# Kernel optimization log

Measured on AMD Instinct MI355X. Metric: run time of the kernel, lower is better.

The kernel has to match this reference:

```python
import jax, jax.numpy as jnp
import numpy as np

INV_COEFF = 25.0
VAR_COEFF = 25.0
COV_COEFF = 1.0


def _cdist(a, b):
    # Euclidean pairwise distance, (B,N,C)x(B,M,C)->(B,N,M)
    a2 = jnp.sum(a * a, axis=-1)[:, :, None]
    b2 = jnp.sum(b * b, axis=-1)[:, None, :]
    d2 = a2 + b2 - 2.0 * jnp.einsum('bnc,bmc->bnm', a, b)
    return jnp.sqrt(jnp.maximum(d2, 0.0))


def _nn_match(input_maps, candidate_maps, distances, num_matches):
    # top-1 NN per input row, then keep the num_matches rows with the
    # smallest NN-distance, preserving original row order (matches the
    # torch sort/sort/mask + masked_select logic exactly).
    min_vals = jnp.min(distances, axis=-1)       # (B, N)
    nn_idx = jnp.argmin(distances, axis=-1)      # (B, N)
    order = jnp.argsort(min_vals, axis=1)[:, :num_matches]   # rows with smallest min-dist
    indices_selected = jnp.sort(order, axis=1)               # restore original order (B, M)
    nn_selected = jnp.take_along_axis(nn_idx, indices_selected, axis=1)  # (B, M)
    filt_in = jnp.take_along_axis(input_maps, indices_selected[..., None], axis=1)
    filt_cand = jnp.take_along_axis(candidate_maps, nn_selected[..., None], axis=1)
    return filt_in, filt_cand


def _vicreg_loss(x, y):
    # x, y: (B, M, C)
    B = x.shape[0]
    C = x.shape[-1]
    repr_loss = INV_COEFF * jnp.mean((x - y) ** 2)
    # gather_center: subtract batch mean (single-device equivalent)
    xc = x - jnp.mean(x, axis=0, keepdims=True)
    yc = y - jnp.mean(y, axis=0, keepdims=True)
    std_x = jnp.sqrt(jnp.var(xc, axis=0, ddof=1) + 1e-4)
    std_y = jnp.sqrt(jnp.var(yc, axis=0, ddof=1) + 1e-4)
    std_loss = VAR_COEFF * (jnp.mean(jax.nn.relu(1.0 - std_x)) / 2
                            + jnp.mean(jax.nn.relu(1.0 - std_y)) / 2)
    # covariance per location: permute to (M, B, C), center over batch
    xp = jnp.transpose(xc, (1, 0, 2))
    yp = jnp.transpose(yc, (1, 0, 2))
    xp = xp - jnp.mean(xp, axis=-2, keepdims=True)
    yp = yp - jnp.mean(yp, axis=-2, keepdims=True)
    cov_x = jnp.einsum('mnc,mnd->mcd', xp, xp) / (B - 1)
    cov_y = jnp.einsum('mnc,mnd->mcd', yp, yp) / (B - 1)
    off = 1.0 - jnp.eye(C, dtype=x.dtype)
    cov_loss = (jnp.sum((cov_x * off) ** 2, axis=(-2, -1)) / C / 2
                + jnp.sum((cov_y * off) ** 2, axis=(-2, -1)) / C / 2)
    cov_loss = COV_COEFF * jnp.mean(cov_loss)
    return repr_loss, std_loss, cov_loss


def _local_loss(maps_1, maps_2, location_1, location_2, num_matches):
    # L2-feature-space NN matching, both directions
    m1f_l2, m1nn_l2 = _nn_match(maps_1, maps_2, _cdist(maps_1, maps_2), num_matches)
    m2f_l2, m2nn_l2 = _nn_match(maps_2, maps_1, _cdist(maps_2, maps_1), num_matches)
    # location-space NN matching, both directions
    loc1 = location_1.reshape(location_1.shape[0], -1, location_1.shape[-1])
    loc2 = location_2.reshape(location_2.shape[0], -1, location_2.shape[-1])
    m1f_loc, m1nn_loc = _nn_match(maps_1, maps_2, _cdist(loc1, loc2), num_matches)
    m2f_loc, m2nn_loc = _nn_match(maps_2, maps_1, _cdist(loc2, loc1), num_matches)
    inv = var = cov = 0.0
    for a, b in ((m1f_l2, m1nn_l2), (m2f_l2, m2nn_l2),
                 (m1f_loc, m1nn_loc), (m2f_loc, m2nn_loc)):
        i, v, c = _vicreg_loss(a, b)
        inv = inv + i
        var = var + v
        cov = cov + c
    return inv + var + cov


def setup_inputs() -> dict:
    key = jax.random.key(0)
    k1, k2, k3, k4 = jax.random.split(key, 4)
    B, HW, C, H = 64, 784, 512, 28
    return {
        'maps_1': jax.random.normal(k1, (B, HW, C), dtype=jnp.float32),
        'maps_2': jax.random.normal(k2, (B, HW, C), dtype=jnp.float32),
        'location_1': jax.random.uniform(k3, (B, H, H, 2), dtype=jnp.float32),
        'location_2': jax.random.uniform(k4, (B, H, H, 2), dtype=jnp.float32),
        'num_matches': 256,
    }


def reference(maps_1, maps_2, location_1, location_2, num_matches):
    return _local_loss(maps_1, maps_2, location_1, location_2, num_matches)
```

## Files before the change

kernel.cpp:

```cpp
#include <hip/hip_runtime.h>
#include <stdint.h>

#define B 64
#define N 784
#define C 512
#define M 256

typedef unsigned long long u64;
typedef unsigned short u16;
typedef __attribute__((ext_vector_type(8))) short short8;
typedef __attribute__((ext_vector_type(4))) float f32x4;

static __device__ __forceinline__ u64 umin64(u64 a, u64 b) { return a < b ? a : b; }

static __device__ __forceinline__ u16 f2bf(float x) {
    unsigned u = __float_as_uint(x);
    return (u16)((u + 0x7FFFu + ((u >> 16) & 1u)) >> 16);
}
static __device__ __forceinline__ float b2f(u16 v) {
    return __uint_as_float((unsigned)v << 16);
}

static __device__ __forceinline__ void gload_lds16(const u16* g, u16* l) {
    __builtin_amdgcn_global_load_lds((const __attribute__((address_space(1))) void*)g,
                                     (__attribute__((address_space(3))) void*)l, 16, 0, 0);
}

__global__ __launch_bounds__(256) void convnorm_kernel(
    const float* __restrict__ m1, const float* __restrict__ m2,
    u16* __restrict__ abf, u16* __restrict__ bbf, float* __restrict__ nrm,
    u64* __restrict__ rowkey) {
    int gid = blockIdx.x * 256 + threadIdx.x;
    if (gid < 2 * B * N) rowkey[gid] = ~0ull;
    int w = blockIdx.x * 4 + (threadIdx.x >> 6);
    int lane = threadIdx.x & 63;
    if (w >= 2 * B * N) return;
    const float* src = (w < B * N) ? m1 : m2;
    u16* dst = (w < B * N) ? abf : bbf;
    int row = (w < B * N) ? w : w - B * N;
    const float4* p = (const float4*)(src + (size_t)row * C);
    u64* q = (u64*)(dst + (size_t)row * C);
    float s = 0.f;
#pragma unroll
    for (int i = 0; i < 2; ++i) {
        int idx = lane + i * 64;
        float4 v = p[idx];
        s += v.x * v.x + v.y * v.y + v.z * v.z + v.w * v.w;
        q[idx] = (u64)f2bf(v.x) | ((u64)f2bf(v.y) << 16) |
                 ((u64)f2bf(v.z) << 32) | ((u64)f2bf(v.w) << 48);
    }
#pragma unroll
    for (int off = 32; off > 0; off >>= 1) s += __shfl_down(s, off, 64);
    if (lane == 0) nrm[w] = s;
}

__global__ __launch_bounds__(256, 2) void feat_mfma_kernel(
    const u16* __restrict__ abf, const u16* __restrict__ bbf,
    const float* __restrict__ nrm, u64* __restrict__ rowkey) {
    int id = blockIdx.x;
    int xcd = id & 7;
    int q = id >> 3;
    int hi = q / 49, t49 = q - hi * 49;
    int b = hi * 8 + xcd;
    int tn = t49 / 7, tm = t49 - tn * 7;

    const int t = threadIdx.x;
    const int lane = t & 63, wv = t >> 6;
    const int wr = wv >> 1, wc = wv & 1;

    __shared__ __align__(16) unsigned char RAW[65536];
    __shared__ float sNa[128], sNb[128];

    const int row0 = tn * 128, col0 = tm * 128;
    if (t < 128) {
        int n = row0 + t;
        sNa[t] = (n < N) ? nrm[b * N + n] : __builtin_inff();
    } else {
        int m = col0 + (t - 128);
        sNb[t - 128] = (m < N) ? nrm[B * N + b * N + m] : __builtin_inff();
    }

    size_t aofs[4], bofs[4];
    int ldso[4];
#pragma unroll
    for (int s = 0; s < 4; ++s) {
        int c = (wv * 4 + s) * 64 + lane;
        int rl = c >> 3;
        int grp = (c & 7) ^ (rl & 7);
        int ga = row0 + rl; if (ga > N - 1) ga = N - 1;
        int gb = col0 + rl; if (gb > N - 1) gb = N - 1;
        aofs[s] = ((size_t)b * N + ga) * C + grp * 8;
        bofs[s] = ((size_t)b * N + gb) * C + grp * 8;
        ldso[s] = (wv * 4 + s) * 512;
    }

    const int l15 = lane & 15;
    const int sA_base = (wr * 64 + l15) * 64;
    const int sB_base = (wc * 64 + l15) * 64;
    const int swz0 = (((lane >> 4) + 0) ^ (l15 & 7)) << 3;
    const int swz1 = (((lane >> 4) + 4) ^ (l15 & 7)) << 3;

    f32x4 acc[4][4];
#pragma unroll
    for (int i = 0; i < 4; ++i)
#pragma unroll
        for (int j = 0; j < 4; ++j) acc[i][j] = (f32x4){0.f, 0.f, 0.f, 0.f};

    {
        u16* A0 = (u16*)RAW;
        u16* B0 = A0 + 8192;
#pragma unroll
        for (int s = 0; s < 4; ++s) {
            gload_lds16(abf + aofs[s], &A0[ldso[s]]);
            gload_lds16(bbf + bofs[s], &B0[ldso[s]]);
        }
    }

    for (int kt = 0; kt < 8; ++kt) {
        const int cur = kt & 1;
        if (kt < 7) {
            int ke = (kt + 1) * 64;
            u16* An = (u16*)(RAW + (cur ^ 1) * 32768);
            u16* Bn = An + 8192;
#pragma unroll
            for (int s = 0; s < 4; ++s) {
                gload_lds16(abf + aofs[s] + ke, &An[ldso[s]]);
                gload_lds16(bbf + bofs[s] + ke, &Bn[ldso[s]]);
            }
            asm volatile("s_waitcnt vmcnt(8)" ::: "memory");
        } else {
            asm volatile("s_waitcnt vmcnt(0)" ::: "memory");
        }
        __builtin_amdgcn_s_barrier();

        const u16* Als = (const u16*)(RAW + cur * 32768);
        const u16* Bls = Als + 8192;
        const u16* pA0 = Als + sA_base + swz0;
        const u16* pA1 = Als + sA_base + swz1;
        const u16* pB0 = Bls + sB_base + swz0;
        const u16* pB1 = Bls + sB_base + swz1;
#pragma unroll
        for (int ks = 0; ks < 2; ++ks) {
            const u16* pA = ks ? pA1 : pA0;
            const u16* pB = ks ? pB1 : pB0;
            short8 afr[4], bfr[4];
#pragma unroll
            for (int f = 0; f < 4; ++f) {
                afr[f] = *(const short8*)(pA + f * 1024);
                bfr[f] = *(const short8*)(pB + f * 1024);
            }
#pragma unroll
            for (int fi = 0; fi < 4; ++fi)
#pragma unroll
                for (int fj = 0; fj < 4; ++fj)
                    acc[fi][fj] = __builtin_amdgcn_mfma_f32_16x16x32_bf16(
                        afr[fi], bfr[fj], acc[fi][fj], 0, 0, 0);
        }
        asm volatile("s_waitcnt lgkmcnt(0)" ::: "memory");
        __builtin_amdgcn_s_barrier();
    }

    const int g4 = (lane >> 4) << 2;
    float na4[4][4], nb4[4];
#pragma unroll
    for (int fi = 0; fi < 4; ++fi) {
        float4 v = *(const float4*)&sNa[wr * 64 + fi * 16 + g4];
        na4[fi][0] = v.x; na4[fi][1] = v.y; na4[fi][2] = v.z; na4[fi][3] = v.w;
    }
#pragma unroll
    for (int fj = 0; fj < 4; ++fj) nb4[fj] = sNb[wc * 64 + fj * 16 + l15];

    u64(*red)[33] = (u64(*)[33])RAW;
    u64 ck[4] = {~0ull, ~0ull, ~0ull, ~0ull};
#pragma unroll
    for (int fi = 0; fi < 4; ++fi) {
        int rl = wr * 64 + fi * 16 + g4;
        u64 rk[4] = {~0ull, ~0ull, ~0ull, ~0ull};
#pragma unroll
        for (int fj = 0; fj < 4; ++fj) {
            unsigned colidx = (unsigned)(col0 + wc * 64 + fj * 16 + l15);
#pragma unroll
            for (int reg = 0; reg < 4; ++reg) {
                float d2 = fmaxf(na4[fi][reg] + nb4[fj] - 2.f * acc[fi][fj][reg], 0.f);
                u64 hv = ((u64)__float_as_uint(d2) << 32);
                rk[reg] = umin64(rk[reg], hv | colidx);
                ck[fj] = umin64(ck[fj], hv | (unsigned)(row0 + rl + reg));
            }
        }
#pragma unroll
        for (int reg = 0; reg < 4; ++reg)
            red[rl + reg][(wc << 4) | l15] = rk[reg];
    }
#pragma unroll
    for (int fj = 0; fj < 4; ++fj) {
        u64 best = ck[fj];
        best = umin64(best, __shfl_xor(best, 16, 64));
        best = umin64(best, __shfl_xor(best, 32, 64));
        if (lane < 16) {
            int m = col0 + wc * 64 + fj * 16 + lane;
            if (m < N) atomicMin(&rowkey[(size_t)B * N + (size_t)b * N + m], best);
        }
    }
    __syncthreads();
    if (t < 128) {
        u64 best = red[t][0];
#pragma unroll
        for (int x = 1; x < 32; ++x) best = umin64(best, red[t][x]);
        int n = row0 + t;
        if (n < N) atomicMin(&rowkey[(size_t)b * N + n], best);
    }
}

__global__ __launch_bounds__(256) void loc_dist_kernel(
    const float* __restrict__ l1, const float* __restrict__ l2,
    u64* __restrict__ rowkey) {
    const int dir = blockIdx.z;
    const int b = blockIdx.y;
    const int t = threadIdx.x;
    const int n = blockIdx.x * 256 + t;
    __shared__ __align__(16) float4 s4[N];
    const float* Ap = dir ? l2 : l1;
    const float* Bp = dir ? l1 : l2;
    for (int i = t; i < N; i += 256) {
        float2 qv = ((const float2*)Bp)[b * N + i];
        s4[i] = make_float4(qv.x, qv.y, qv.x * qv.x + qv.y * qv.y, 0.f);
    }
    __syncthreads();
    if (n >= N) return;
    float2 a = ((const float2*)Ap)[b * N + n];
    float a2 = a.x * a.x + a.y * a.y;
    float nax = -2.f * a.x, nay = -2.f * a.y;
    u64 best = ~0ull;
#pragma unroll 4
    for (int mm = 0; mm < N; ++mm) {
        float4 v = s4[mm];
        float d2 = fmaxf(fmaf(nax, v.x, fmaf(nay, v.y, a2 + v.z)), 0.f);
        u64 kv = ((u64)__float_as_uint(d2) << 32) | (unsigned)mm;
        best = kv < best ? kv : best;
    }
    rowkey[(size_t)(2 + dir) * B * N + (size_t)b * N + n] = best;
}

__global__ __launch_bounds__(256) void select_kernel(
    const u64* __restrict__ rowkey, int* __restrict__ sel_idx,
    int* __restrict__ nn_idx, float* __restrict__ acc) {
    const int b = blockIdx.x;
    const int dir = blockIdx.y;
    const int t = threadIdx.x;
    if (b == 0 && dir == 0 && t < 8) acc[t] = 0.f;
    __shared__ u64 sk[1024];
    const u64* rk = rowkey + (size_t)dir * B * N + (size_t)b * N;
    for (int i = t; i < 1024; i += 256)
        sk[i] = (i < N) ? ((rk[i] & 0xFFFFFFFF00000000ull) | (unsigned)i) : ~0ull;
    __syncthreads();
    for (unsigned k = 2; k <= 1024; k <<= 1) {
        for (unsigned j = k >> 1; j > 0; j >>= 1) {
            for (unsigned i = t; i < 1024; i += 256) {
                unsigned ixj = i ^ j;
                if (ixj > i) {
                    u64 x = sk[i], y = sk[ixj];
                    bool up = ((i & k) == 0);
                    if ((x > y) == up) { sk[i] = y; sk[ixj] = x; }
                }
            }
            __syncthreads();
        }
    }
    unsigned myidx = (unsigned)(sk[t] & 0xFFFFFFFFull);
    __syncthreads();
    unsigned* si = (unsigned*)sk;
    si[t] = myidx;
    __syncthreads();
    for (unsigned k = 2; k <= 256; k <<= 1) {
        for (unsigned j = k >> 1; j > 0; j >>= 1) {
            unsigned i = t, ixj = i ^ j;
            if (ixj > i) {
                unsigned x = si[i], y = si[ixj];
                bool up = ((i & k) == 0);
                if ((x > y) == up) { si[i] = y; si[ixj] = x; }
            }
            __syncthreads();
        }
    }
    int sel = (int)si[t];
    sel_idx[((size_t)dir * B + b) * M + t] = sel;
    nn_idx[((size_t)dir * B + b) * M + t] = (int)(unsigned)(rk[sel] & 0xFFFFFFFFull);
}

__global__ __launch_bounds__(512, 1) void vicreg_mfma_kernel(
    const u16* __restrict__ abf, const u16* __restrict__ bbf,
    const int* __restrict__ sel_idx, const int* __restrict__ nn_idx,
    float* __restrict__ acc, float* __restrict__ outp) {
    const int mloc = blockIdx.x;
    const int p = blockIdx.y;
    const int t = threadIdx.x;
    const int l = t & 63, w = t >> 6;
    const int kh = w >> 2, wl = w & 3;

    __shared__ __align__(16) u16 Xs[4][64 * 128];
    __shared__ __align__(16) u16 Ys[4][64 * 128];
    __shared__ float colpart[2][4][4][128];
    __shared__ float Rsx[64], Rsy[64];
    __shared__ int xi[64], yi[64];
    __shared__ float redsc[4][4];

    if (t < 64) xi[t] = sel_idx[((size_t)p * B + t) * M + mloc];
    else if (t < 128) yi[t - 64] = nn_idx[((size_t)p * B + (t - 64)) * M + mloc];
    __syncthreads();

    const u16* Xg = (p & 1) ? bbf : abf;
    const u16* Yg = (p & 1) ? abf : bbf;
    unsigned xofs[4], yofs[4];
    int ldst[4];
#pragma unroll
    for (int s = 0; s < 4; ++s) {
        int r = wl * 16 + s * 4 + (l >> 4);
        int cs = (l & 15) ^ (r & 15);
        xofs[s] = (unsigned)((r * N + xi[r]) * C + cs * 8);
        yofs[s] = (unsigned)((r * N + yi[r]) * C + cs * 8);
        ldst[s] = (wl * 16 + s * 4) * 128;
    }

#pragma unroll
    for (int cc = 0; cc < 2; ++cc) {
        int kc = 2 * kh + cc;
#pragma unroll
        for (int s = 0; s < 4; ++s) {
            gload_lds16(Xg + xofs[s] + kc * 128, &Xs[kc][ldst[s]]);
            gload_lds16(Yg + yofs[s] + kc * 128, &Ys[kc][ldst[s]]);
        }
    }
    __syncthreads();

    f32x4 Gx[4], Gy[4], Z;
#pragma unroll
    for (int j = 0; j < 4; ++j) { Gx[j] = (f32x4){0,0,0,0}; Gy[j] = (f32x4){0,0,0,0}; }
    Z = (f32x4){0, 0, 0, 0};
    float stdacc = 0.f, covdacc = 0.f, reprp = 0.f;

#pragma unroll
    for (int cc = 0; cc < 2; ++cc) {
        const int kc = 2 * kh + cc;
        const u16* Xc = Xs[kc];
        const u16* Yc = Ys[kc];

#pragma unroll
        for (int ks = 0; ks < 4; ++ks) {
            int cb = ks * 4 + (l >> 4);
            int pe = (cb ^ (l & 15)) << 3;
            short8 ax = *(const short8*)&Xc[((wl << 4) + (l & 15)) * 128 + pe];
            short8 ay = *(const short8*)&Yc[((wl << 4) + (l & 15)) * 128 + pe];
            short8 bx[4], by[4];
#pragma unroll
            for (int j = 0; j < 4; ++j) {
                bx[j] = *(const short8*)&Xc[(j * 16 + (l & 15)) * 128 + pe];
                by[j] = *(const short8*)&Yc[(j * 16 + (l & 15)) * 128 + pe];
            }
#pragma unroll
            for (int j = 0; j < 4; ++j) {
                Gx[j] = __builtin_amdgcn_mfma_f32_16x16x32_bf16(ax, bx[j], Gx[j], 0, 0, 0);
                Gy[j] = __builtin_amdgcn_mfma_f32_16x16x32_bf16(ay, by[j], Gy[j], 0, 0, 0);
            }
            Z = __builtin_amdgcn_mfma_f32_16x16x32_bf16(ax, ay, Z, 0, 0, 0);
        }

        {
            int c4 = (l & 31) << 2;
            int cc8 = c4 >> 3, h = (c4 >> 2) & 1;
            int g2 = (wl << 1) + (l >> 5);
            float s1x0 = 0, s1x1 = 0, s1x2 = 0, s1x3 = 0;
            float s2x0 = 0, s2x1 = 0, s2x2 = 0, s2x3 = 0;
            float s1y0 = 0, s1y1 = 0, s1y2 = 0, s1y3 = 0;
            float s2y0 = 0, s2y1 = 0, s2y2 = 0, s2y3 = 0;
#pragma unroll
            for (int rr = 0; rr < 8; ++rr) {
                int r = g2 * 8 + rr;
                int off = r * 128 + ((cc8 ^ (r & 15)) << 3) + h * 4;
                ushort4 vx = *(const ushort4*)&Xc[off];
                ushort4 vy = *(const ushort4*)&Yc[off];
                float x0 = b2f(vx.x), x1 = b2f(vx.y), x2 = b2f(vx.z), x3 = b2f(vx.w);
                float y0 = b2f(vy.x), y1 = b2f(vy.y), y2 = b2f(vy.z), y3 = b2f(vy.w);
                s1x0 += x0; s1x1 += x1; s1x2 += x2; s1x3 += x3;
                s2x0 = fmaf(x0, x0, s2x0); s2x1 = fmaf(x1, x1, s2x1);
                s2x2 = fmaf(x2, x2, s2x2); s2x3 = fmaf(x3, x3, s2x3);
                s1y0 += y0; s1y1 += y1; s1y2 += y2; s1y3 += y3;
                s2y0 = fmaf(y0, y0, s2y0); s2y1 = fmaf(y1, y1, s2y1);
                s2y2 = fmaf(y2, y2, s2y2); s2y3 = fmaf(y3, y3, s2y3);
            }
            s1x0 += __shfl_xor(s1x0, 32, 64); s1x1 += __shfl_xor(s1x1, 32, 64);
            s1x2 += __shfl_xor(s1x2, 32, 64); s1x3 += __shfl_xor(s1x3, 32, 64);
            s2x0 += __shfl_xor(s2x0, 32, 64); s2x1 += __shfl_xor(s2x1, 32, 64);
            s2x2 += __shfl_xor(s2x2, 32, 64); s2x3 += __shfl_xor(s2x3, 32, 64);
            s1y0 += __shfl_xor(s1y0, 32, 64); s1y1 += __shfl_xor(s1y1, 32, 64);
            s1y2 += __shfl_xor(s1y2, 32, 64); s1y3 += __shfl_xor(s1y3, 32, 64);
            s2y0 += __shfl_xor(s2y0, 32, 64); s2y1 += __shfl_xor(s2y1, 32, 64);
            s2y2 += __shfl_xor(s2y2, 32, 64); s2y3 += __shfl_xor(s2y3, 32, 64);
            if (l < 32) {
                *(float4*)&colpart[kh][wl][0][c4] = make_float4(s1x0, s1x1, s1x2, s1x3);
                *(float4*)&colpart[kh][wl][1][c4] = make_float4(s2x0, s2x1, s2x2, s2x3);
                *(float4*)&colpart[kh][wl][2][c4] = make_float4(s1y0, s1y1, s1y2, s1y3);
                *(float4*)&colpart[kh][wl][3][c4] = make_float4(s2y0, s2y1, s2y2, s2y3);
            }
        }
        __syncthreads();

        if (t < 256) {
            int khp = t >> 7, col = t & 127;
            float s1x = 0, s2x = 0, s1y = 0, s2y = 0;
#pragma unroll
            for (int ww = 0; ww < 4; ++ww) {
                s1x += colpart[khp][ww][0][col]; s2x += colpart[khp][ww][1][col];
                s1y += colpart[khp][ww][2][col]; s2y += colpart[khp][ww][3][col];
            }
            float sx = s2x - s1x * s1x * (1.f / 64.f);
            float sy = s2y - s1y * s1y * (1.f / 64.f);
            stdacc += fmaxf(0.f, 1.f - sqrtf(sx * (1.f / 63.f) + 1e-4f)) +
                      fmaxf(0.f, 1.f - sqrtf(sy * (1.f / 63.f) + 1e-4f));
            covdacc += sx * sx + sy * sy;
            reprp += s2x + s2y;
        }
        __syncthreads();
    }

    {
        float* ex = (float*)&Xs[0][0];
        int base = ((wl << 6) + l) * 36;
        if (kh == 1) {
#pragma unroll
            for (int j = 0; j < 4; ++j)
#pragma unroll
                for (int reg = 0; reg < 4; ++reg) {
                    ex[base + j * 4 + reg] = Gx[j][reg];
                    ex[base + 16 + j * 4 + reg] = Gy[j][reg];
                }
#pragma unroll
            for (int reg = 0; reg < 4; ++reg) ex[base + 32 + reg] = Z[reg];
        }
        __syncthreads();
        if (kh == 0) {
#pragma unroll
            for (int j = 0; j < 4; ++j)
#pragma unroll
                for (int reg = 0; reg < 4; ++reg) {
                    Gx[j][reg] += ex[base + j * 4 + reg];
                    Gy[j][reg] += ex[base + 16 + j * 4 + reg];
                }
#pragma unroll
            for (int reg = 0; reg < 4; ++reg) Z[reg] += ex[base + 32 + reg];
        }
    }

    float zd = 0.f;
    float rsx[4] = {0, 0, 0, 0}, rsy[4] = {0, 0, 0, 0};
    if (kh == 0) {
        int rbase = (l >> 4) << 2, col = l & 15;
#pragma unroll
        for (int reg = 0; reg < 4; ++reg)
            zd += (col == rbase + reg) ? Z[reg] : 0.f;
#pragma unroll
        for (int reg = 0; reg < 4; ++reg) {
            rsx[reg] = Gx[0][reg] + Gx[1][reg] + Gx[2][reg] + Gx[3][reg];
            rsy[reg] = Gy[0][reg] + Gy[1][reg] + Gy[2][reg] + Gy[3][reg];
        }
#pragma unroll
        for (int off = 1; off < 16; off <<= 1)
#pragma unroll
            for (int reg = 0; reg < 4; ++reg) {
                rsx[reg] += __shfl_xor(rsx[reg], off, 64);
                rsy[reg] += __shfl_xor(rsy[reg], off, 64);
            }
        if ((l & 15) == 0) {
#pragma unroll
            for (int reg = 0; reg < 4; ++reg) {
                Rsx[(wl << 4) + ((l >> 4) << 2) + reg] = rsx[reg];
                Rsy[(wl << 4) + ((l >> 4) << 2) + reg] = rsy[reg];
            }
        }
    }
    __syncthreads();
    if (kh == 0) {
        float myx = Rsx[l], myy = Rsy[l];
#pragma unroll
        for (int off = 1; off < 64; off <<= 1) {
            myx += __shfl_xor(myx, off, 64);
            myy += __shfl_xor(myy, off, 64);
        }
        float tX = myx * (1.f / 4096.f), tY = myy * (1.f / 4096.f);
        float kn = 0.f;
#pragma unroll
        for (int j = 0; j < 4; ++j) {
            float cX = Rsx[(j << 4) + (l & 15)] * (1.f / 64.f);
            float cY = Rsy[(j << 4) + (l & 15)] * (1.f / 64.f);
#pragma unroll
            for (int reg = 0; reg < 4; ++reg) {
                float K1 = Gx[j][reg] - rsx[reg] * (1.f / 64.f) - cX + tX;
                kn = fmaf(K1, K1, kn);
                float K2 = Gy[j][reg] - rsy[reg] * (1.f / 64.f) - cY + tY;
                kn = fmaf(K2, K2, kn);
            }
        }
        float v0 = reprp - 2.f * zd, v1 = stdacc, v2 = covdacc, v3 = kn;
#pragma unroll
        for (int off = 1; off < 64; off <<= 1) {
            v0 += __shfl_xor(v0, off, 64);
            v1 += __shfl_xor(v1, off, 64);
            v2 += __shfl_xor(v2, off, 64);
            v3 += __shfl_xor(v3, off, 64);
        }
        if (l == 0) { redsc[wl][0] = v0; redsc[wl][1] = v1;
                      redsc[wl][2] = v2; redsc[wl][3] = v3; }
    }
    __syncthreads();
    if (t == 0) {
        float r0 = 0, r1 = 0, r2 = 0, r3 = 0;
#pragma unroll
        for (int ww = 0; ww < 4; ++ww) {
            r0 += redsc[ww][0]; r1 += redsc[ww][1];
            r2 += redsc[ww][2]; r3 += redsc[ww][3];
        }
        atomicAdd(&acc[0], r0);
        atomicAdd(&acc[1], r1);
        atomicAdd(&acc[2], r3 - r2);
        __threadfence();
        unsigned old = atomicAdd((unsigned*)&acc[6], 1u);
        if (old == 4 * M - 1) {
            float a0 = atomicAdd(&acc[0], 0.f);
            float a1 = atomicAdd(&acc[1], 0.f);
            float a2 = atomicAdd(&acc[2], 0.f);
            float repr = 25.f * a0 / ((float)B * (float)M * (float)C);
            float stdl = 12.5f * a1 / ((float)M * (float)C);
            float cov = a2 / (63.f * 63.f * (float)C * 2.f) / (float)M;
            outp[0] = repr + stdl + cov;
        }
    }
}

__global__ __launch_bounds__(256) void init_kernel(u64* rowkey, float* acc) {
    int i = blockIdx.x * 256 + threadIdx.x;
    if (i < 4 * B * N) rowkey[i] = ~0ull;
    if (i < 8) acc[i] = 0.f;
}

__global__ __launch_bounds__(256) void norms_kernel(const float* __restrict__ m1,
                                                    const float* __restrict__ m2,
                                                    float* __restrict__ nrm) {
    int w = blockIdx.x * 4 + (threadIdx.x >> 6);
    int lane = threadIdx.x & 63;
    if (w >= 2 * B * N) return;
    const float* src = (w < B * N) ? m1 : m2;
    int row = (w < B * N) ? w : w - B * N;
    const float4* p = (const float4*)(src + (size_t)row * C);
    float s = 0.f;
#pragma unroll
    for (int i = 0; i < 2; ++i) {
        float4 v = p[lane + i * 64];
        s += v.x * v.x + v.y * v.y + v.z * v.z + v.w * v.w;
    }
#pragma unroll
    for (int off = 32; off > 0; off >>= 1) s += __shfl_down(s, off, 64);
    if (lane == 0) nrm[w] = s;
}

__global__ __launch_bounds__(256) void feat_dist_kernel(
    const float* __restrict__ m1, const float* __restrict__ m2,
    const float* __restrict__ nrm, u64* __restrict__ rowkey) {
    const int b = blockIdx.z;
    const int tn = blockIdx.x, tm = blockIdx.y;
    __shared__ float As[64][68];
    __shared__ float Bt[64][68];
    __shared__ u64 red[64][16];
    const int t = threadIdx.x;
    const int ty = t >> 4, tx = t & 15;
    float acc[4][4] = {};
    const float* A = m1 + (size_t)b * N * C;
    const float* Bm = m2 + (size_t)b * N * C;

    for (int k0 = 0; k0 < C; k0 += 64) {
#pragma unroll
        for (int it = 0; it < 4; ++it) {
            int idx = t + it * 256;
            int r = idx >> 4, cc = (idx & 15) << 2;
            int n = tn * 64 + r;
            float4 v = make_float4(0.f, 0.f, 0.f, 0.f);
            if (n < N) v = *(const float4*)(A + (size_t)n * C + k0 + cc);
            *(float4*)&As[r][cc] = v;
            int mm = tm * 64 + r;
            float4 w = make_float4(0.f, 0.f, 0.f, 0.f);
            if (mm < N) w = *(const float4*)(Bm + (size_t)mm * C + k0 + cc);
            Bt[cc + 0][r] = w.x; Bt[cc + 1][r] = w.y;
            Bt[cc + 2][r] = w.z; Bt[cc + 3][r] = w.w;
        }
        __syncthreads();
#pragma unroll 4
        for (int kq = 0; kq < 64; kq += 4) {
            float aa[4][4], bb[4][4];
#pragma unroll
            for (int i = 0; i < 4; ++i) {
                float4 v = *(const float4*)&As[ty * 4 + i][kq];
                aa[i][0] = v.x; aa[i][1] = v.y; aa[i][2] = v.z; aa[i][3] = v.w;
            }
#pragma unroll
            for (int qq = 0; qq < 4; ++qq) {
                float4 v = *(const float4*)&Bt[kq + qq][tx * 4];
                bb[qq][0] = v.x; bb[qq][1] = v.y; bb[qq][2] = v.z; bb[qq][3] = v.w;
            }
#pragma unroll
            for (int qq = 0; qq < 4; ++qq)
#pragma unroll
                for (int i = 0; i < 4; ++i)
#pragma unroll
                    for (int j = 0; j < 4; ++j)
                        acc[i][j] = fmaf(aa[i][qq], bb[qq][j], acc[i][j]);
        }
        __syncthreads();
    }

    u64 rk[4] = {~0ull, ~0ull, ~0ull, ~0ull};
    u64 ck[4] = {~0ull, ~0ull, ~0ull, ~0ull};
    const float* nr1 = nrm;
    const float* nr2 = nrm + B * N;
#pragma unroll
    for (int i = 0; i < 4; ++i) {
        int n = tn * 64 + ty * 4 + i;
        if (n >= N) continue;
        float a2 = nr1[b * N + n];
#pragma unroll
        for (int j = 0; j < 4; ++j) {
            int mm = tm * 64 + tx * 4 + j;
            if (mm >= N) continue;
            float b2 = nr2[b * N + mm];
            float d2 = a2 + b2 - 2.f * acc[i][j];
            unsigned vb = __float_as_uint(fmaxf(d2, 0.f));
            u64 kv = ((u64)vb << 32);
            rk[i] = umin64(rk[i], kv | (unsigned)mm);
            ck[j] = umin64(ck[j], kv | (unsigned)n);
        }
    }
#pragma unroll
    for (int i = 0; i < 4; ++i) red[ty * 4 + i][tx] = rk[i];
    __syncthreads();
    if (t < 64) {
        u64 best = red[t][0];
#pragma unroll
        for (int x = 1; x < 16; ++x) best = umin64(best, red[t][x]);
        int n = tn * 64 + t;
        if (n < N && best != ~0ull)
            atomicMin(&rowkey[(size_t)b * N + n], best);
    }
    __syncthreads();
#pragma unroll
    for (int j = 0; j < 4; ++j) red[tx * 4 + j][ty] = ck[j];
    __syncthreads();
    if (t < 64) {
        u64 best = red[t][0];
#pragma unroll
        for (int x = 1; x < 16; ++x) best = umin64(best, red[t][x]);
        int mm = tm * 64 + t;
        if (mm < N && best != ~0ull)
            atomicMin(&rowkey[(size_t)B * N + (size_t)b * N + mm], best);
    }
}

__device__ __forceinline__ float blockReduce(float v, float* redb, int t) {
    __syncthreads();
    redb[t] = v;
    __syncthreads();
    for (int s = 128; s > 0; s >>= 1) {
        if (t < s) redb[t] += redb[t + s];
        __syncthreads();
    }
    return redb[0];
}

__global__ __launch_bounds__(256) void vicreg_kernel(
    const float* __restrict__ m1, const float* __restrict__ m2,
    const int* __restrict__ sel_idx, const int* __restrict__ nn_idx,
    float* __restrict__ acc) {
    const int mloc = blockIdx.x;
    const int p = blockIdx.y;
    const int t = threadIdx.x;
    const float* X = (p & 1) ? m2 : m1;
    const float* Y = (p & 1) ? m1 : m2;
    __shared__ float Xs[64][65];
    __shared__ float Ys[64][65];
    __shared__ int xi[64], yi[64];
    __shared__ float pst[192][5];
    __shared__ float Rs[64];
    __shared__ float Tsh;
    __shared__ float redb[256];

    if (t < 64) {
        xi[t] = sel_idx[((size_t)p * B + t) * M + mloc];
        yi[t] = nn_idx[((size_t)p * B + t) * M + mloc];
    }
    __syncthreads();

    float Gx[4][4] = {}, Gy[4][4] = {};
    float stdx = 0, stdy = 0, covdx = 0, covdy = 0, repr = 0;
    const int i0 = (t >> 4) << 2, j0 = (t & 15) << 2;

    for (int c0 = 0; c0 < C; c0 += 64) {
#pragma unroll
        for (int it = 0; it < 4; ++it) {
            int fidx = t + it * 256;
            int r = fidx >> 4, cc = (fidx & 15) << 2;
            float4 v = *(const float4*)(X + ((size_t)r * N + xi[r]) * C + c0 + cc);
            Xs[r][cc] = v.x; Xs[r][cc + 1] = v.y; Xs[r][cc + 2] = v.z; Xs[r][cc + 3] = v.w;
            float4 w = *(const float4*)(Y + ((size_t)r * N + yi[r]) * C + c0 + cc);
            Ys[r][cc] = w.x; Ys[r][cc + 1] = w.y; Ys[r][cc + 2] = w.z; Ys[r][cc + 3] = w.w;
        }
        __syncthreads();
#pragma unroll 4
        for (int k = 0; k < 64; ++k) {
            float ax[4], bx[4], ay[4], by[4];
#pragma unroll
            for (int i = 0; i < 4; ++i) { ax[i] = Xs[i0 + i][k]; ay[i] = Ys[i0 + i][k]; }
#pragma unroll
            for (int j = 0; j < 4; ++j) { bx[j] = Xs[j0 + j][k]; by[j] = Ys[j0 + j][k]; }
#pragma unroll
            for (int i = 0; i < 4; ++i)
#pragma unroll
                for (int j = 0; j < 4; ++j) {
                    Gx[i][j] = fmaf(ax[i], bx[j], Gx[i][j]);
                    Gy[i][j] = fmaf(ay[i], by[j], Gy[i][j]);
                }
        }
        {
            float s1x = 0, s2x = 0, s1y = 0, s2y = 0, sxy = 0;
            int col = t & 63, g = t >> 6;
            for (int r = g * 16; r < g * 16 + 16; ++r) {
                float xv = Xs[r][col], yv = Ys[r][col];
                s1x += xv; s2x += xv * xv;
                s1y += yv; s2y += yv * yv;
                sxy += xv * yv;
            }
            if (g) {
                float* qq = pst[(g - 1) * 64 + col];
                qq[0] = s1x; qq[1] = s2x; qq[2] = s1y; qq[3] = s2y; qq[4] = sxy;
            }
            __syncthreads();
            if (g == 0) {
#pragma unroll
                for (int gg = 0; gg < 3; ++gg) {
                    float* qq = pst[gg * 64 + col];
                    s1x += qq[0]; s2x += qq[1]; s1y += qq[2]; s2y += qq[3]; sxy += qq[4];
                }
                float xb = s1x * (1.f / 64.f);
                float sx = s2x - 64.f * xb * xb;
                float yb = s1y * (1.f / 64.f);
                float sy = s2y - 64.f * yb * yb;
                stdx += fmaxf(0.f, 1.f - sqrtf(sx * (1.f / 63.f) + 1e-4f));
                stdy += fmaxf(0.f, 1.f - sqrtf(sy * (1.f / 63.f) + 1e-4f));
                covdx += sx * sx;
                covdy += sy * sy;
                repr += s2x + s2y - 2.f * sxy;
            }
            __syncthreads();
        }
    }

    float knx = 0.f, kny = 0.f;
    float (*Gs)[65] = (float(*)[65]) & Xs[0][0];
    __syncthreads();
#pragma unroll
    for (int i = 0; i < 4; ++i)
#pragma unroll
        for (int j = 0; j < 4; ++j) Gs[i0 + i][j0 + j] = Gx[i][j];
    __syncthreads();
    if (t < 64) {
        float r = 0;
        for (int j = 0; j < 64; ++j) r += Gs[t][j];
        Rs[t] = r;
    }
    __syncthreads();
    if (t < 64) {
        float r = Rs[t];
#pragma unroll
        for (int off = 32; off > 0; off >>= 1) r += __shfl_down(r, off, 64);
        if (t == 0) Tsh = r;
    }
    __syncthreads();
    {
        float T = Tsh * (1.f / 4096.f);
#pragma unroll
        for (int i = 0; i < 4; ++i)
#pragma unroll
            for (int j = 0; j < 4; ++j) {
                float Kij = Gx[i][j] - (Rs[i0 + i] + Rs[j0 + j]) * (1.f / 64.f) + T;
                knx = fmaf(Kij, Kij, knx);
            }
    }
    __syncthreads();
#pragma unroll
    for (int i = 0; i < 4; ++i)
#pragma unroll
        for (int j = 0; j < 4; ++j) Gs[i0 + i][j0 + j] = Gy[i][j];
    __syncthreads();
    if (t < 64) {
        float r = 0;
        for (int j = 0; j < 64; ++j) r += Gs[t][j];
        Rs[t] = r;
    }
    __syncthreads();
    if (t < 64) {
        float r = Rs[t];
#pragma unroll
        for (int off = 32; off > 0; off >>= 1) r += __shfl_down(r, off, 64);
        if (t == 0) Tsh = r;
    }
    __syncthreads();
    {
        float T = Tsh * (1.f / 4096.f);
#pragma unroll
        for (int i = 0; i < 4; ++i)
#pragma unroll
            for (int j = 0; j < 4; ++j) {
                float Kij = Gy[i][j] - (Rs[i0 + i] + Rs[j0 + j]) * (1.f / 64.f) + T;
                kny = fmaf(Kij, Kij, kny);
            }
    }

    float v_repr = blockReduce(repr, redb, t);
    float v_std = blockReduce(stdx + stdy, redb, t);
    float v_covd = blockReduce(covdx + covdy, redb, t);
    float v_kn = blockReduce(knx + kny, redb, t);
    if (t == 0) {
        atomicAdd(&acc[0], v_repr);
        atomicAdd(&acc[1], v_std);
        atomicAdd(&acc[2], v_kn - v_covd);
    }
}

__global__ void finalize_kernel(const float* __restrict__ acc, float* __restrict__ out) {
    if (threadIdx.x == 0 && blockIdx.x == 0) {
        float repr = 25.f * acc[0] / ((float)B * (float)M * (float)C);
        float stdl = 12.5f * acc[1] / ((float)M * (float)C);
        float cov = acc[2] / (63.f * 63.f * (float)C * 2.f) / (float)M;
        out[0] = repr + stdl + cov;
    }
}

extern "C" void kernel_launch(void* const* d_in, const int* in_sizes, int n_in,
                              void* d_out, int out_size, void* d_ws, size_t ws_size,
                              hipStream_t stream) {
    const float* m1 = (const float*)d_in[0];
    const float* m2 = (const float*)d_in[1];
    const float* l1 = (const float*)d_in[2];
    const float* l2 = (const float*)d_in[3];
    float* out = (float*)d_out;
    char* ws = (char*)d_ws;

    u64* rowkey = (u64*)ws;
    size_t off = (size_t)4 * B * N * sizeof(u64);
    float* nrm = (float*)(ws + off); off += (size_t)2 * B * N * sizeof(float);
    int* sel_idx = (int*)(ws + off); off += (size_t)4 * B * M * sizeof(int);
    int* nn_idx = (int*)(ws + off);  off += (size_t)4 * B * M * sizeof(int);
    float* acc = (float*)(ws + off); off += 256;
    off = (off + 255) & ~(size_t)255;
    u16* abf = (u16*)(ws + off);
    u16* bbf = abf + (size_t)B * N * C;
    size_t need = off + (size_t)2 * B * N * C * sizeof(u16);
    bool use_mfma = ws_size >= need;

    if (use_mfma) {
        convnorm_kernel<<<dim3(2 * B * N / 4), dim3(256), 0, stream>>>(
            m1, m2, abf, bbf, nrm, rowkey);
        feat_mfma_kernel<<<dim3(64 * 49), dim3(256), 0, stream>>>(abf, bbf, nrm, rowkey);
        loc_dist_kernel<<<dim3((N + 255) / 256, B, 2), dim3(256), 0, stream>>>(l1, l2, rowkey);
        select_kernel<<<dim3(B, 4), dim3(256), 0, stream>>>(rowkey, sel_idx, nn_idx, acc);
        vicreg_mfma_kernel<<<dim3(M, 4), dim3(512), 0, stream>>>(
            abf, bbf, sel_idx, nn_idx, acc, out);
    } else {
        init_kernel<<<dim3((4 * B * N + 255) / 256), dim3(256), 0, stream>>>(rowkey, acc);
        norms_kernel<<<dim3(2 * B * N / 4), dim3(256), 0, stream>>>(m1, m2, nrm);
        feat_dist_kernel<<<dim3(13, 13, B), dim3(256), 0, stream>>>(m1, m2, nrm, rowkey);
        loc_dist_kernel<<<dim3((N + 255) / 256, B, 2), dim3(256), 0, stream>>>(l1, l2, rowkey);
        select_kernel<<<dim3(B, 4), dim3(256), 0, stream>>>(rowkey, sel_idx, nn_idx, acc);
        vicreg_kernel<<<dim3(M, 4), dim3(256), 0, stream>>>(m1, m2, sel_idx, nn_idx, acc);
        finalize_kernel<<<dim3(1), dim3(64), 0, stream>>>(acc, out);
    }
}
```

Baseline: 265.9 us.

## Add FP8 copy of feature maps and FP8 MFMA VICReg kernel

The conversion kernel now also writes an FP8 copy of both feature maps when the workspace is large enough. The final VICReg stage then gathers the selected rows from that FP8 copy and computes the Gram and cross products with fp8 MFMA on 256-thread blocks. This halves the gather traffic and LDS footprint of that stage. The price is an extra full-size FP8 write in the conversion kernel, plus reduced precision in the variance and covariance terms, which may push results outside tolerance.

```diff
diff --git a/kernel.cpp b/kernel.cpp
--- a/kernel.cpp
+++ b/kernel.cpp
@@ -8,6 +8,8 @@
 
 typedef unsigned long long u64;
 typedef unsigned short u16;
+typedef unsigned char u8;
+typedef long i64;
 typedef __attribute__((ext_vector_type(8))) short short8;
 typedef __attribute__((ext_vector_type(4))) float f32x4;
 
@@ -25,11 +27,16 @@
     __builtin_amdgcn_global_load_lds((const __attribute__((address_space(1))) void*)g,
                                      (__attribute__((address_space(3))) void*)l, 16, 0, 0);
 }
+static __device__ __forceinline__ void gload_lds16b(const u8* g, u8* l) {
+    __builtin_amdgcn_global_load_lds((const __attribute__((address_space(1))) void*)g,
+                                     (__attribute__((address_space(3))) void*)l, 16, 0, 0);
+}
 
 __global__ __launch_bounds__(256) void convnorm_kernel(
     const float* __restrict__ m1, const float* __restrict__ m2,
-    u16* __restrict__ abf, u16* __restrict__ bbf, float* __restrict__ nrm,
-    u64* __restrict__ rowkey) {
+    u16* __restrict__ abf, u16* __restrict__ bbf,
+    u8* __restrict__ a8, u8* __restrict__ b8,
+    float* __restrict__ nrm, u64* __restrict__ rowkey, int do8) {
     int gid = blockIdx.x * 256 + threadIdx.x;
     if (gid < 2 * B * N) rowkey[gid] = ~0ull;
     int w = blockIdx.x * 4 + (threadIdx.x >> 6);
@@ -37,9 +44,11 @@
     if (w >= 2 * B * N) return;
     const float* src = (w < B * N) ? m1 : m2;
     u16* dst = (w < B * N) ? abf : bbf;
+    u8* dst8 = (w < B * N) ? a8 : b8;
     int row = (w < B * N) ? w : w - B * N;
     const float4* p = (const float4*)(src + (size_t)row * C);
     u64* q = (u64*)(dst + (size_t)row * C);
+    unsigned* q8 = (unsigned*)(dst8 + (size_t)row * C);
     float s = 0.f;
 #pragma unroll
     for (int i = 0; i < 2; ++i) {
@@ -48,6 +57,11 @@
         s += v.x * v.x + v.y * v.y + v.z * v.z + v.w * v.w;
         q[idx] = (u64)f2bf(v.x) | ((u64)f2bf(v.y) << 16) |
                  ((u64)f2bf(v.z) << 32) | ((u64)f2bf(v.w) << 48);
+        if (do8) {
+            int pk = __builtin_amdgcn_cvt_pk_fp8_f32(v.x, v.y, 0, false);
+            pk = __builtin_amdgcn_cvt_pk_fp8_f32(v.z, v.w, pk, true);
+            q8[idx] = (unsigned)pk;
+        }
     }
 #pragma unroll
     for (int off = 32; off > 0; off >>= 1) s += __shfl_down(s, off, 64);
@@ -287,6 +301,227 @@
     nn_idx[((size_t)dir * B + b) * M + t] = (int)(unsigned)(rk[sel] & 0xFFFFFFFFull);
 }
 
+__global__ __launch_bounds__(256, 2) void vicreg_fp8_kernel(
+    const u8* __restrict__ a8, const u8* __restrict__ b8,
+    const int* __restrict__ sel_idx, const int* __restrict__ nn_idx,
+    float* __restrict__ acc, float* __restrict__ outp) {
+    const int mloc = blockIdx.x;
+    const int p = blockIdx.y;
+    const int t = threadIdx.x;
+    const int l = t & 63, w = t >> 6;
+
+    __shared__ __align__(16) u8 X8[4][64 * 128];
+    __shared__ __align__(16) u8 Y8[4][64 * 128];
+    __shared__ float colpart[4][4][128];
+    __shared__ float Rsx[64], Rsy[64];
+    __shared__ int xi[64], yi[64];
+    __shared__ float redsc[4][4];
+
+    if (t < 64) xi[t] = sel_idx[((size_t)p * B + t) * M + mloc];
+    else if (t < 128) yi[t - 64] = nn_idx[((size_t)p * B + (t - 64)) * M + mloc];
+    __syncthreads();
+
+    const u8* Xg = (p & 1) ? b8 : a8;
+    const u8* Yg = (p & 1) ? a8 : b8;
+    size_t xofs[2], yofs[2];
+    int ldst[2];
+#pragma unroll
+    for (int s = 0; s < 2; ++s) {
+        int r = w * 16 + s * 8 + (l >> 3);
+        int sg = (l & 7) ^ (r & 7);
+        xofs[s] = ((size_t)(r * N + xi[r])) * C + sg * 16;
+        yofs[s] = ((size_t)(r * N + yi[r])) * C + sg * 16;
+        ldst[s] = (w * 16 + s * 8) * 128;
+    }
+
+#pragma unroll
+    for (int kc = 0; kc < 4; ++kc)
+#pragma unroll
+        for (int s = 0; s < 2; ++s) {
+            gload_lds16b(Xg + xofs[s] + kc * 128, &X8[kc][ldst[s]]);
+            gload_lds16b(Yg + yofs[s] + kc * 128, &Y8[kc][ldst[s]]);
+        }
+    __syncthreads();
+
+    f32x4 Gx[4], Gy[4], Z;
+#pragma unroll
+    for (int j = 0; j < 4; ++j) { Gx[j] = (f32x4){0,0,0,0}; Gy[j] = (f32x4){0,0,0,0}; }
+    Z = (f32x4){0, 0, 0, 0};
+    float stdacc = 0.f, covdacc = 0.f, reprp = 0.f;
+
+#pragma unroll
+    for (int kc = 0; kc < 4; ++kc) {
+        const u8* Xc = X8[kc];
+        const u8* Yc = Y8[kc];
+
+#pragma unroll
+        for (int ks = 0; ks < 4; ++ks) {
+            int g = (ks << 1) + ((l >> 4) >> 1);
+            int wi = ((l >> 4) & 1) << 3;
+            int soff = ((g ^ (l & 7)) << 4) + wi;
+            int ra = (w << 4) + (l & 15);
+            i64 ax = *(const i64*)&Xc[ra * 128 + soff];
+            i64 ay = *(const i64*)&Yc[ra * 128 + soff];
+            i64 bx[4], by[4];
+#pragma unroll
+            for (int j = 0; j < 4; ++j) {
+                int rb = (j << 4) + (l & 15);
+                bx[j] = *(const i64*)&Xc[rb * 128 + soff];
+                by[j] = *(const i64*)&Yc[rb * 128 + soff];
+            }
+#pragma unroll
+            for (int j = 0; j < 4; ++j) {
+                Gx[j] = __builtin_amdgcn_mfma_f32_16x16x32_fp8_fp8(ax, bx[j], Gx[j], 0, 0, 0);
+                Gy[j] = __builtin_amdgcn_mfma_f32_16x16x32_fp8_fp8(ay, by[j], Gy[j], 0, 0, 0);
+            }
+            Z = __builtin_amdgcn_mfma_f32_16x16x32_fp8_fp8(ax, ay, Z, 0, 0, 0);
+        }
+
+        {
+            int c4 = (l & 31) << 2;
+            int g2 = (w << 1) + (l >> 5);
+            float s1x0 = 0, s1x1 = 0, s1x2 = 0, s1x3 = 0;
+            float s2x0 = 0, s2x1 = 0, s2x2 = 0, s2x3 = 0;
+            float s1y0 = 0, s1y1 = 0, s1y2 = 0, s1y3 = 0;
+            float s2y0 = 0, s2y1 = 0, s2y2 = 0, s2y3 = 0;
+#pragma unroll
+            for (int rr = 0; rr < 8; ++rr) {
+                int r = g2 * 8 + rr;
+                int off = r * 128 + (((c4 >> 4) ^ (r & 7)) << 4) + (c4 & 15);
+                unsigned wx = *(const unsigned*)&Xc[off];
+                unsigned wy = *(const unsigned*)&Yc[off];
+                float x0 = __builtin_amdgcn_cvt_f32_fp8(wx, 0);
+                float x1 = __builtin_amdgcn_cvt_f32_fp8(wx, 1);
+                float x2 = __builtin_amdgcn_cvt_f32_fp8(wx, 2);
+                float x3 = __builtin_amdgcn_cvt_f32_fp8(wx, 3);
+                float y0 = __builtin_amdgcn_cvt_f32_fp8(wy, 0);
+                float y1 = __builtin_amdgcn_cvt_f32_fp8(wy, 1);
+                float y2 = __builtin_amdgcn_cvt_f32_fp8(wy, 2);
+                float y3 = __builtin_amdgcn_cvt_f32_fp8(wy, 3);
+                s1x0 += x0; s1x1 += x1; s1x2 += x2; s1x3 += x3;
+                s2x0 = fmaf(x0, x0, s2x0); s2x1 = fmaf(x1, x1, s2x1);
+                s2x2 = fmaf(x2, x2, s2x2); s2x3 = fmaf(x3, x3, s2x3);
+                s1y0 += y0; s1y1 += y1; s1y2 += y2; s1y3 += y3;
+                s2y0 = fmaf(y0, y0, s2y0); s2y1 = fmaf(y1, y1, s2y1);
+                s2y2 = fmaf(y2, y2, s2y2); s2y3 = fmaf(y3, y3, s2y3);
+            }
+            s1x0 += __shfl_xor(s1x0, 32, 64); s1x1 += __shfl_xor(s1x1, 32, 64);
+            s1x2 += __shfl_xor(s1x2, 32, 64); s1x3 += __shfl_xor(s1x3, 32, 64);
+            s2x0 += __shfl_xor(s2x0, 32, 64); s2x1 += __shfl_xor(s2x1, 32, 64);
+            s2x2 += __shfl_xor(s2x2, 32, 64); s2x3 += __shfl_xor(s2x3, 32, 64);
+            s1y0 += __shfl_xor(s1y0, 32, 64); s1y1 += __shfl_xor(s1y1, 32, 64);
+            s1y2 += __shfl_xor(s1y2, 32, 64); s1y3 += __shfl_xor(s1y3, 32, 64);
+            s2y0 += __shfl_xor(s2y0, 32, 64); s2y1 += __shfl_xor(s2y1, 32, 64);
+            s2y2 += __shfl_xor(s2y2, 32, 64); s2y3 += __shfl_xor(s2y3, 32, 64);
+            if (l < 32) {
+                *(float4*)&colpart[w][0][c4] = make_float4(s1x0, s1x1, s1x2, s1x3);
+                *(float4*)&colpart[w][1][c4] = make_float4(s2x0, s2x1, s2x2, s2x3);
+                *(float4*)&colpart[w][2][c4] = make_float4(s1y0, s1y1, s1y2, s1y3);
+                *(float4*)&colpart[w][3][c4] = make_float4(s2y0, s2y1, s2y2, s2y3);
+            }
+        }
+        __syncthreads();
+
+        if (t < 128) {
+            float s1x = 0, s2x = 0, s1y = 0, s2y = 0;
+#pragma unroll
+            for (int ww = 0; ww < 4; ++ww) {
+                s1x += colpart[ww][0][t]; s2x += colpart[ww][1][t];
+                s1y += colpart[ww][2][t]; s2y += colpart[ww][3][t];
+            }
+            float sx = s2x - s1x * s1x * (1.f / 64.f);
+            float sy = s2y - s1y * s1y * (1.f / 64.f);
+            stdacc += fmaxf(0.f, 1.f - sqrtf(sx * (1.f / 63.f) + 1e-4f)) +
+                      fmaxf(0.f, 1.f - sqrtf(sy * (1.f / 63.f) + 1e-4f));
+            covdacc += sx * sx + sy * sy;
+            reprp += s2x + s2y;
+        }
+        __syncthreads();
+    }
+
+    float zd = 0.f;
+    {
+        int rbase = (l >> 4) << 2, col = l & 15;
+#pragma unroll
+        for (int reg = 0; reg < 4; ++reg)
+            zd += (col == rbase + reg) ? Z[reg] : 0.f;
+    }
+    float rsx[4], rsy[4];
+#pragma unroll
+    for (int reg = 0; reg < 4; ++reg) {
+        rsx[reg] = Gx[0][reg] + Gx[1][reg] + Gx[2][reg] + Gx[3][reg];
+        rsy[reg] = Gy[0][reg] + Gy[1][reg] + Gy[2][reg] + Gy[3][reg];
+    }
+#pragma unroll
+    for (int off = 1; off < 16; off <<= 1)
+#pragma unroll
+        for (int reg = 0; reg < 4; ++reg) {
+            rsx[reg] += __shfl_xor(rsx[reg], off, 64);
+            rsy[reg] += __shfl_xor(rsy[reg], off, 64);
+        }
+    if ((l & 15) == 0) {
+#pragma unroll
+        for (int reg = 0; reg < 4; ++reg) {
+            Rsx[(w << 4) + ((l >> 4) << 2) + reg] = rsx[reg];
+            Rsy[(w << 4) + ((l >> 4) << 2) + reg] = rsy[reg];
+        }
+    }
+    __syncthreads();
+    float myx = Rsx[l], myy = Rsy[l];
+#pragma unroll
+    for (int off = 1; off < 64; off <<= 1) {
+        myx += __shfl_xor(myx, off, 64);
+        myy += __shfl_xor(myy, off, 64);
+    }
+    float tX = myx * (1.f / 4096.f), tY = myy * (1.f / 4096.f);
+    float kn = 0.f;
+#pragma unroll
+    for (int j = 0; j < 4; ++j) {
+        float cX = Rsx[(j << 4) + (l & 15)] * (1.f / 64.f);
+        float cY = Rsy[(j << 4) + (l & 15)] * (1.f / 64.f);
+#pragma unroll
+        for (int reg = 0; reg < 4; ++reg) {
+            float K1 = Gx[j][reg] - rsx[reg] * (1.f / 64.f) - cX + tX;
+            kn = fmaf(K1, K1, kn);
+            float K2 = Gy[j][reg] - rsy[reg] * (1.f / 64.f) - cY + tY;
+            kn = fmaf(K2, K2, kn);
+        }
+    }
+
+    float v0 = reprp - 2.f * zd, v1 = stdacc, v2 = covdacc, v3 = kn;
+#pragma unroll
+    for (int off = 1; off < 64; off <<= 1) {
+        v0 += __shfl_xor(v0, off, 64);
+        v1 += __shfl_xor(v1, off, 64);
+        v2 += __shfl_xor(v2, off, 64);
+        v3 += __shfl_xor(v3, off, 64);
+    }
+    if (l == 0) { redsc[w][0] = v0; redsc[w][1] = v1; redsc[w][2] = v2; redsc[w][3] = v3; }
+    __syncthreads();
+    if (t == 0) {
+        float r0 = 0, r1 = 0, r2 = 0, r3 = 0;
+#pragma unroll
+        for (int ww = 0; ww < 4; ++ww) {
+            r0 += redsc[ww][0]; r1 += redsc[ww][1];
+            r2 += redsc[ww][2]; r3 += redsc[ww][3];
+        }
+        atomicAdd(&acc[0], r0);
+        atomicAdd(&acc[1], r1);
+        atomicAdd(&acc[2], r3 - r2);
+        __threadfence();
+        unsigned old = atomicAdd((unsigned*)&acc[6], 1u);
+        if (old == 4 * M - 1) {
+            float a0 = atomicAdd(&acc[0], 0.f);
+            float a1 = atomicAdd(&acc[1], 0.f);
+            float a2 = atomicAdd(&acc[2], 0.f);
+            float repr = 25.f * a0 / ((float)B * (float)M * (float)C);
+            float stdl = 12.5f * a1 / ((float)M * (float)C);
+            float cov = a2 / (63.f * 63.f * (float)C * 2.f) / (float)M;
+            outp[0] = repr + stdl + cov;
+        }
+    }
+}
+
 __global__ __launch_bounds__(512, 1) void vicreg_mfma_kernel(
     const u16* __restrict__ abf, const u16* __restrict__ bbf,
     const int* __restrict__ sel_idx, const int* __restrict__ nn_idx,
@@ -343,7 +578,6 @@
         const int kc = 2 * kh + cc;
         const u16* Xc = Xs[kc];
         const u16* Yc = Ys[kc];
-
 #pragma unroll
         for (int ks = 0; ks < 4; ++ks) {
             int cb = ks * 4 + (l >> 4);
@@ -363,7 +597,6 @@
             }
             Z = __builtin_amdgcn_mfma_f32_16x16x32_bf16(ax, ay, Z, 0, 0, 0);
         }
-
         {
             int c4 = (l & 31) << 2;
             int cc8 = c4 >> 3, h = (c4 >> 2) & 1;
@@ -403,7 +636,6 @@
             }
         }
         __syncthreads();
-
         if (t < 256) {
             int khp = t >> 7, col = t & 127;
             float s1x = 0, s2x = 0, s1y = 0, s2y = 0;
@@ -860,16 +1092,25 @@
     u16* abf = (u16*)(ws + off);
     u16* bbf = abf + (size_t)B * N * C;
     size_t need = off + (size_t)2 * B * N * C * sizeof(u16);
+    u8* a8 = (u8*)(ws + need);
+    u8* b8 = a8 + (size_t)B * N * C;
+    size_t need8 = need + (size_t)2 * B * N * C;
     bool use_mfma = ws_size >= need;
+    bool use_fp8 = ws_size >= need8;
 
     if (use_mfma) {
         convnorm_kernel<<<dim3(2 * B * N / 4), dim3(256), 0, stream>>>(
-            m1, m2, abf, bbf, nrm, rowkey);
+            m1, m2, abf, bbf, a8, b8, nrm, rowkey, (int)use_fp8);
         feat_mfma_kernel<<<dim3(64 * 49), dim3(256), 0, stream>>>(abf, bbf, nrm, rowkey);
         loc_dist_kernel<<<dim3((N + 255) / 256, B, 2), dim3(256), 0, stream>>>(l1, l2, rowkey);
         select_kernel<<<dim3(B, 4), dim3(256), 0, stream>>>(rowkey, sel_idx, nn_idx, acc);
-        vicreg_mfma_kernel<<<dim3(M, 4), dim3(512), 0, stream>>>(
-            abf, bbf, sel_idx, nn_idx, acc, out);
+        if (use_fp8) {
+            vicreg_fp8_kernel<<<dim3(M, 4), dim3(256), 0, stream>>>(
+                a8, b8, sel_idx, nn_idx, acc, out);
+        } else {
+            vicreg_mfma_kernel<<<dim3(M, 4), dim3(512), 0, stream>>>(
+                abf, bbf, sel_idx, nn_idx, acc, out);
+        }
     } else {
         init_kernel<<<dim3((4 * B * N + 255) / 256), dim3(256), 0, stream>>>(rowkey, acc);
         norms_kernel<<<dim3(2 * B * N / 4), dim3(256), 0, stream>>>(m1, m2, nrm);
```

Result: slower. 276.1 us (+3.9%).
